# Kernel optimization log

Hardware: AMD Instinct MI355X
Metric: run time of the kernel (lower is better)

Reference implementation:

```python
import jax, jax.numpy as jnp
import numpy as np

H = 256; EMB = 256; MAX_POS = 20; NBOND = 4; ATOM = 40
DEPTH_T = 5; DEPTH_G = 5
NT, MT = 8000, 16000      # tree nodes / tree messages
NA, MA = 25000, 50000     # atoms / bond messages
NB = 6; NC = 12; NROOT = 256
VC, VI = 5000, 15000      # cluster / inter vocab sizes

FLOAT_KEYS = ("E_c","E_i","Wc_w","Wc_b","Wi_w","Wi_b","Wroot_w","Wroot_b",
  "t_Wo_w","t_Wo_b","t_Wz_w","t_Wz_b","t_Wr_w","t_Ur_w","t_Ur_b","t_Wh_w","t_Wh_b",
  "i_Wo_w","i_Wo_b","i_Wz_w","i_Wz_b","i_Wr_w","i_Ur_w","i_Ur_b","i_Wh_w","i_Wh_b",
  "g_Wo_w","g_Wo_b","g_Wz_w","g_Wz_b","g_Wr_w","g_Ur_w","g_Ur_b","g_Wh_w","g_Wh_b")
INT_KEYS = ("t_fnode","t_fmess","t_agraph","t_bgraph","t_cgraph",
            "g_fnode","g_fmess","g_agraph","g_bgraph","roots")

def _gru(fmess, bgraph, Wz_w, Wz_b, Wr_w, Ur_w, Ur_b, Wh_w, Wh_b, depth):
    # depth-iterated GRU message passing; row 0 of h is padding (kept at zero).
    M, F = fmess.shape
    Hs = Wz_w.shape[1]
    mask = jnp.ones((M, 1), fmess.dtype).at[0, 0].set(0.0)
    # loop-invariant input projections (W_z/W_h split along concat axis)
    fz = fmess @ Wz_w[:F] + Wz_b
    fr = fmess @ Wr_w
    fh = fmess @ Wh_w[:F] + Wh_b
    Wz_h, Wh_h = Wz_w[F:], Wh_w[F:]
    def step(h, _):
        h_nei = h[bgraph]                       # [M, B, H] irregular gather
        sum_h = h_nei.sum(1)
        z = jax.nn.sigmoid(fz + sum_h @ Wz_h)
        r = jax.nn.sigmoid(fr[:, None, :] + h_nei @ Ur_w + Ur_b)
        sum_gh = (r * h_nei).sum(1)
        pre_h = jnp.tanh(fh + sum_gh @ Wh_h)
        h_new = ((1.0 - z) * sum_h + z * pre_h) * mask
        return h_new, None
    h0 = jnp.zeros((M, Hs), fmess.dtype)
    h, _ = jax.lax.scan(step, h0, None, length=depth)
    return h

def _mpn(fnode, fmess, agraph, bgraph, p, depth):
    h = _gru(fmess, bgraph, p["Wz_w"], p["Wz_b"], p["Wr_w"], p["Ur_w"], p["Ur_b"], p["Wh_w"], p["Wh_b"], depth)
    nei = h[agraph].sum(1)                      # index_select_ND + sum
    nh = jax.nn.relu(jnp.concatenate([fnode, nei], 1) @ p["Wo_w"] + p["Wo_b"])
    return nh.at[0].set(0.0), h                 # zero padding row (mask)

def _enc_params(fl, pre):
    return {k: fl[pre + k] for k in ("Wo_w","Wo_b","Wz_w","Wz_b","Wr_w","Ur_w","Ur_b","Wh_w","Wh_b")}

def _forward(fl, it):
    E_pos = jnp.eye(MAX_POS, dtype=jnp.float32)
    E_a = jnp.eye(ATOM, dtype=jnp.float32)
    E_b = jnp.eye(NBOND, dtype=jnp.float32)
    t_fnode, t_fmess = it["t_fnode"], it["t_fmess"]
    g_fnode, g_fmess = it["g_fnode"], it["g_fmess"]
    # ---- embed_graph + graph_encoder ----
    g_hnode = E_a[g_fnode]                                           # [NA, ATOM] one-hot
    g_hmess = jnp.concatenate([g_hnode[g_fmess[:, 0]], E_b[g_fmess[:, 2]], E_pos[g_fmess[:, 3]]], 1)
    hatom, _ = _mpn(g_hnode, g_hmess, it["g_agraph"], it["g_bgraph"], _enc_params(fl, "g_"), DEPTH_G)
    # ---- embed_inter + inter_encoder ----
    fin = fl["E_i"][t_fnode[:, 1]]
    hn = hatom[it["t_cgraph"]].sum(1)                                # cluster <- atoms
    hn = jax.nn.relu(jnp.concatenate([fin, hn], 1) @ fl["Wi_w"] + fl["Wi_b"])
    hm = jnp.concatenate([hn[t_fmess[:, 0]], E_pos[t_fmess[:, 2]]], 1)
    hinter, _ = _mpn(hn, hm, it["t_agraph"], it["t_bgraph"], _enc_params(fl, "i_"), DEPTH_T)
    # ---- embed_tree + tree_encoder ----
    fin = fl["E_c"][t_fnode[:, 0]]
    hn = jax.nn.relu(jnp.concatenate([fin, hinter], 1) @ fl["Wc_w"] + fl["Wc_b"])
    hm = jnp.concatenate([hn[t_fmess[:, 0]], E_pos[t_fmess[:, 2]]], 1)
    htree, h_msg = _mpn(hn, hm, it["t_agraph"], it["t_bgraph"], _enc_params(fl, "t_"), DEPTH_T)
    # ---- embed_root: uses pre-encoder node embedding hn and message states h_msg ----
    r = it["roots"]
    nei = h_msg[it["t_agraph"][r]].sum(1)
    hroot = jnp.tanh(jnp.concatenate([hn[r], nei], 1) @ fl["Wroot_w"] + fl["Wroot_b"])
    return hroot, htree, hinter, hatom

def setup_inputs() -> dict:
    ki = iter(jax.random.split(jax.random.key(0), 80))
    def nk():
        return next(ki)
    ri = jax.random.randint
    rn = lambda shape: 0.08 * jax.random.normal(nk(), shape, jnp.float32)
    inp = {}
    inp["t_fnode"] = ri(nk(), (NT, 2), 0, VC)
    inp["t_fmess"] = jnp.stack([ri(nk(), (MT,), 0, NT), ri(nk(), (MT,), 0, NT), ri(nk(), (MT,), 0, MAX_POS)], 1)
    inp["t_agraph"] = ri(nk(), (NT, NB), 0, MT)
    inp["t_bgraph"] = ri(nk(), (MT, NB), 0, MT)
    inp["t_cgraph"] = ri(nk(), (NT, NC), 0, NA)
    inp["g_fnode"] = ri(nk(), (NA,), 0, ATOM)
    inp["g_fmess"] = jnp.stack([ri(nk(), (MA,), 0, NA), ri(nk(), (MA,), 0, NA), ri(nk(), (MA,), 0, NBOND), ri(nk(), (MA,), 0, MAX_POS)], 1)
    inp["g_agraph"] = ri(nk(), (NA, NB), 0, MA)
    inp["g_bgraph"] = ri(nk(), (MA, NB), 0, MA)
    inp["roots"] = ri(nk(), (NROOT,), 0, NT)
    inp["E_c"] = rn((VC, EMB)); inp["E_i"] = rn((VI, EMB))
    inp["Wc_w"] = rn((EMB + H, H)); inp["Wc_b"] = rn((H,))
    inp["Wi_w"] = rn((EMB + H, H)); inp["Wi_b"] = rn((H,))
    inp["Wroot_w"] = rn((2 * H, H)); inp["Wroot_b"] = rn((H,))
    for pre, in_sz, nf in (("t_", H + MAX_POS, H), ("i_", H + MAX_POS, H), ("g_", ATOM + NBOND + MAX_POS, ATOM)):
        inp[pre + "Wo_w"] = rn((nf + H, H)); inp[pre + "Wo_b"] = rn((H,))
        inp[pre + "Wz_w"] = rn((in_sz + H, H)); inp[pre + "Wz_b"] = rn((H,))
        inp[pre + "Wr_w"] = rn((in_sz, H))
        inp[pre + "Ur_w"] = rn((H, H)); inp[pre + "Ur_b"] = rn((H,))
        inp[pre + "Wh_w"] = rn((in_sz + H, H)); inp[pre + "Wh_b"] = rn((H,))
    return inp

def reference(E_c, E_i, Wc_w, Wc_b, Wi_w, Wi_b, Wroot_w, Wroot_b,
              t_Wo_w, t_Wo_b, t_Wz_w, t_Wz_b, t_Wr_w, t_Ur_w, t_Ur_b, t_Wh_w, t_Wh_b,
              i_Wo_w, i_Wo_b, i_Wz_w, i_Wz_b, i_Wr_w, i_Ur_w, i_Ur_b, i_Wh_w, i_Wh_b,
              g_Wo_w, g_Wo_b, g_Wz_w, g_Wz_b, g_Wr_w, g_Ur_w, g_Ur_b, g_Wh_w, g_Wh_b,
              t_fnode, t_fmess, t_agraph, t_bgraph, t_cgraph,
              g_fnode, g_fmess, g_agraph, g_bgraph, roots):
    a = dict(locals())
    fl = {k: a[k] for k in FLOAT_KEYS}
    it = {k: a[k] for k in INT_KEYS}
    return _forward(fl, it)
```

## Files before the change

kernel.cpp:

```cpp
#include <hip/hip_runtime.h>
#include <hip/hip_bf16.h>
#include <math.h>

typedef __hip_bfloat16 bf16;
typedef __attribute__((ext_vector_type(8))) short  bf16x8;
typedef __attribute__((ext_vector_type(4))) float  f32x4;

#define NT_ 8000
#define MT_ 16000
#define NA_ 25000
#define MA_ 50000
#define NROOT_ 256

struct Feat {
  const float* dtab; const int* didx; int dstride;
  const float* otab;
  const int* oidx0; int os0; int oo0;
  const int* oidx1; int os1; int oo1;
  const int* oidx2; int os2; int oo2;
  const float* bias;
};

__device__ __forceinline__ float rcpf_(float x){ return __builtin_amdgcn_rcpf(x); }
__device__ __forceinline__ float sigm(float x){ return rcpf_(1.0f + __expf(-x)); }
__device__ __forceinline__ float tanh_f(float x){
  float t = __expf(2.0f*x);
  return 1.0f - 2.0f*rcpf_(t + 1.0f);
}

__device__ __forceinline__ float ubf(unsigned int u){ union{unsigned int i; float f;} x; x.i = u<<16; return x.f; }
__device__ __forceinline__ unsigned int pack2bf(float a, float b){
  bf16 x = __float2bfloat16(a), y = __float2bfloat16(b);
  unsigned short ux = *(unsigned short*)&x, uy = *(unsigned short*)&y;
  return (unsigned int)ux | ((unsigned int)uy<<16);
}
__device__ __forceinline__ short f2bf_s(float f){
  bf16 b = __float2bfloat16(f);
  return *(short*)&b;
}
__device__ __forceinline__ float bfs2f(short s){ return ubf((unsigned short)s); }

__device__ __forceinline__ void acc4(float4& v, const float* p){
  float4 t = *(const float4*)p;
  v.x+=t.x; v.y+=t.y; v.z+=t.z; v.w+=t.w;
}
__device__ __forceinline__ float4 feat_eval4(const Feat& f, int m, int n){
  float4 v = make_float4(0,0,0,0);
  if (f.bias) acc4(v, f.bias + n);
  if (f.dtab) acc4(v, f.dtab + (size_t)f.didx[(size_t)m*f.dstride]*256 + n);
  if (f.otab){
    acc4(v, f.otab + (size_t)(f.oidx0[(size_t)m*f.os0]+f.oo0)*256 + n);
    if (f.oidx1) acc4(v, f.otab + (size_t)(f.oidx1[(size_t)m*f.os1]+f.oo1)*256 + n);
    if (f.oidx2) acc4(v, f.otab + (size_t)(f.oidx2[(size_t)m*f.os2]+f.oo2)*256 + n);
  }
  return v;
}
__device__ __forceinline__ float feat_eval(const Feat& f, int m, int n){
  float v = 0.0f;
  if (f.bias) v += f.bias[n];
  if (f.dtab) v += f.dtab[(size_t)f.didx[(size_t)m*f.dstride]*256 + n];
  if (f.otab){
    v += f.otab[((size_t)(f.oidx0[(size_t)m*f.os0]+f.oo0))*256 + n];
    if (f.oidx1) v += f.otab[((size_t)(f.oidx1[(size_t)m*f.os1]+f.oo1))*256 + n];
    if (f.oidx2) v += f.otab[((size_t)(f.oidx2[(size_t)m*f.os2]+f.oo2))*256 + n];
  }
  return v;
}

__global__ void k_aidx(const int* __restrict__ g_fnode, const int* __restrict__ g_fmess,
                       int* __restrict__ aidx, int M){
  int m = blockIdx.x*blockDim.x + threadIdx.x;
  if (m<M) aidx[m] = g_fnode[g_fmess[(size_t)m*4]];
}

struct SJob { const float* src; short* dst; int nrow; int pad; };
struct SJobs { SJob j[26]; };
__global__ void k_splitw_b(SJobs js){
  SJob jb = js.j[blockIdx.y];
  int idx = blockIdx.x*256 + threadIdx.x;
  if (idx >= jb.nrow*256) return;
  int k = idx>>8, n = idx&255;
  float w = jb.src[idx];
  int base = (((k>>5)*16 + (n>>4))<<10) + (((n&15) + (((k>>3)&3)<<4))<<4) + (k&7);
  short h = f2bf_s(w);
  jb.dst[base]   = h;
  jb.dst[base+8] = f2bf_s(w - bfs2f(h));
}

__global__ void k_gsum4(const float* __restrict__ src, const int* __restrict__ idx,
                        const int* __restrict__ rowsel, int J, int istride,
                        float* __restrict__ dst, int M){
  int wid = (blockIdx.x<<2) + (threadIdx.x>>6);
  if (wid>=M) return;
  int c = (threadIdx.x&63)<<2;
  int r = rowsel ? rowsel[wid] : wid;
  float4 s = make_float4(0,0,0,0);
  for (int j=0;j<J;j++){
    int id = idx[(size_t)r*istride+j];
    acc4(s, src + (size_t)id*256 + c);
  }
  *(float4*)(dst + (size_t)wid*256 + c) = s;
}

__device__ __forceinline__ void build_a(const float* p, bf16x8& hi, bf16x8& lo){
  float4 v0 = *(const float4*)p;
  float4 v1 = *(const float4*)(p+4);
  float vv[8]={v0.x,v0.y,v0.z,v0.w,v1.x,v1.y,v1.z,v1.w};
  #pragma unroll
  for (int j=0;j<8;j++){
    short h = f2bf_s(vv[j]);
    hi[j]=h;
    lo[j]=f2bf_s(vv[j]-bfs2f(h));
  }
}

#define MFMA __builtin_amdgcn_mfma_f32_16x16x32_bf16

__global__ __launch_bounds__(256)
void mfma_mm(const float* __restrict__ A, const short* __restrict__ Bp,
             float* __restrict__ outf, int M)
{
  const int tid=threadIdx.x, lane=tid&63, wc=tid>>6;
  const int rbase = blockIdx.x<<5;
  const int r0 = rbase + (lane&15), r1 = r0 + 16;
  const int koff = (lane>>4)<<3;
  f32x4 zero = {0.f,0.f,0.f,0.f};
  f32x4 acc[2][4];
  #pragma unroll
  for (int rf=0;rf<2;rf++)
    #pragma unroll
    for (int t=0;t<4;t++) acc[rf][t]=zero;

  for (int kc=0;kc<8;kc++){
    bf16x8 a0h={0,0,0,0,0,0,0,0}, a0l=a0h, a1h=a0h, a1l=a0h;
    if (r0<M) build_a(A + (size_t)r0*256 + kc*32 + koff, a0h, a0l);
    if (r1<M) build_a(A + (size_t)r1*256 + kc*32 + koff, a1h, a1l);
    #pragma unroll
    for (int t=0;t<4;t++){
      const short* p = Bp + (((kc<<4)+(wc<<2)+t)<<10) + (lane<<4);
      bf16x8 bh = *(const bf16x8*)p;
      bf16x8 bl = *(const bf16x8*)(p+8);
      acc[0][t]=MFMA(a0h,bh,acc[0][t],0,0,0);
      acc[1][t]=MFMA(a1h,bh,acc[1][t],0,0,0);
      acc[0][t]=MFMA(a0l,bh,acc[0][t],0,0,0);
      acc[1][t]=MFMA(a1l,bh,acc[1][t],0,0,0);
      acc[0][t]=MFMA(a0h,bl,acc[0][t],0,0,0);
      acc[1][t]=MFMA(a1h,bl,acc[1][t],0,0,0);
    }
  }
  const int rr = rbase + ((lane>>4)<<2);
  const int cl = lane&15;
  #pragma unroll
  for (int rf=0;rf<2;rf++)
    #pragma unroll
    for (int t=0;t<4;t++){
      int col = (((wc<<2)+t)<<4) + cl;
      #pragma unroll
      for (int r=0;r<4;r++){
        int m = rr + rf*16 + r;
        if (m<M) outf[(size_t)m*256+col] = acc[rf][t][r];
      }
    }
}

template<int NG>
__global__ __launch_bounds__(256)
void mfma_proj(const float* __restrict__ A1, const int* __restrict__ a1idx, int a1s,
               const float* __restrict__ A2,
               const short* __restrict__ B1p, const short* __restrict__ B2p,
               float* __restrict__ outf, float* __restrict__ outf2,
               Feat f1, int mask0, int M)
{
  const int tid=threadIdx.x, lane=tid&63, wc=tid>>6;
  const int rbase = blockIdx.x<<5;
  const int r0 = rbase + (lane&15), r1 = r0 + 16;
  const int koff = (lane>>4)<<3;
  const float* p0 = (r0<M) ? A1 + (size_t)(a1idx? a1idx[(size_t)r0*a1s] : r0)*256 : nullptr;
  const float* p1 = (r1<M) ? A1 + (size_t)(a1idx? a1idx[(size_t)r1*a1s] : r1)*256 : nullptr;
  f32x4 zero = {0.f,0.f,0.f,0.f};
  f32x4 acc[2][4];
  #pragma unroll
  for (int rf=0;rf<2;rf++)
    #pragma unroll
    for (int t=0;t<4;t++) acc[rf][t]=zero;

  for (int kc=0;kc<8;kc++){
    bf16x8 a0h={0,0,0,0,0,0,0,0}, a0l=a0h, a1h=a0h, a1l=a0h;
    bf16x8 c0h=a0h, c0l=a0h, c1h=a0h, c1l=a0h;
    if (p0) build_a(p0 + kc*32 + koff, a0h, a0l);
    if (p1) build_a(p1 + kc*32 + koff, a1h, a1l);
    if (NG==2){
      if (r0<M) build_a(A2 + (size_t)r0*256 + kc*32 + koff, c0h, c0l);
      if (r1<M) build_a(A2 + (size_t)r1*256 + kc*32 + koff, c1h, c1l);
    }
    #pragma unroll
    for (int t=0;t<4;t++){
      const short* p = B1p + (((kc<<4)+(wc<<2)+t)<<10) + (lane<<4);
      bf16x8 bh = *(const bf16x8*)p;
      bf16x8 bl = *(const bf16x8*)(p+8);
      acc[0][t]=MFMA(a0h,bh,acc[0][t],0,0,0);
      acc[1][t]=MFMA(a1h,bh,acc[1][t],0,0,0);
      acc[0][t]=MFMA(a0l,bh,acc[0][t],0,0,0);
      acc[1][t]=MFMA(a1l,bh,acc[1][t],0,0,0);
      acc[0][t]=MFMA(a0h,bl,acc[0][t],0,0,0);
      acc[1][t]=MFMA(a1h,bl,acc[1][t],0,0,0);
      if (NG==2){
        const short* q = B2p + (((kc<<4)+(wc<<2)+t)<<10) + (lane<<4);
        bf16x8 dh = *(const bf16x8*)q;
        bf16x8 dl = *(const bf16x8*)(q+8);
        acc[0][t]=MFMA(c0h,dh,acc[0][t],0,0,0);
        acc[1][t]=MFMA(c1h,dh,acc[1][t],0,0,0);
        acc[0][t]=MFMA(c0l,dh,acc[0][t],0,0,0);
        acc[1][t]=MFMA(c1l,dh,acc[1][t],0,0,0);
        acc[0][t]=MFMA(c0h,dl,acc[0][t],0,0,0);
        acc[1][t]=MFMA(c1h,dl,acc[1][t],0,0,0);
      }
    }
  }
  const int rr = rbase + ((lane>>4)<<2);
  const int cl = lane&15;
  #pragma unroll
  for (int rf=0;rf<2;rf++)
    #pragma unroll
    for (int t=0;t<4;t++){
      int col = (((wc<<2)+t)<<4) + cl;
      #pragma unroll
      for (int r=0;r<4;r++){
        int m = rr + rf*16 + r;
        if (m>=M) continue;
        float v = acc[rf][t][r] + feat_eval(f1, m, col);
        v = fmaxf(v, 0.0f);
        if (mask0 && m==0) v = 0.0f;
        outf[(size_t)m*256+col] = v;
        if (outf2) outf2[(size_t)m*256+col] = v;
      }
    }
}

__global__ __launch_bounds__(256)
void k_step1hu(Feat fz, Feat fh, const short* __restrict__ Bu,
               float* __restrict__ hout, bf16* __restrict__ hUout, int M)
{
  __shared__ short Hs[32][264];
  const int tid=threadIdx.x, lane=tid&63, wc=tid>>6;
  const int rbase = blockIdx.x<<5;
  const int rr = (lane>>4)<<2;
  const int cl = lane&15;
  const int koff = (lane>>4)<<3;

  #pragma unroll
  for (int rf=0;rf<2;rf++)
    #pragma unroll
    for (int t=0;t<4;t++){
      int col = (((wc<<2)+t)<<4) + cl;
      #pragma unroll
      for (int r=0;r<4;r++){
        int lrow = rr + rf*16 + r;
        int m = rbase + lrow;
        float v = 0.f;
        if (m<M && m!=0)
          v = sigm(feat_eval(fz,m,col))*tanh_f(feat_eval(fh,m,col));
        if (m<M) hout[(size_t)m*256+col]=v;
        Hs[lrow][col]=f2bf_s(v);
      }
    }
  __syncthreads();
  const int r0l = lane&15, r1l = r0l+16;
  f32x4 zero = {0.f,0.f,0.f,0.f};
  f32x4 acc[2][4];
  #pragma unroll
  for (int rf=0;rf<2;rf++)
    #pragma unroll
    for (int t=0;t<4;t++) acc[rf][t]=zero;
  for (int kc=0;kc<8;kc++){
    bf16x8 a0 = *(const bf16x8*)&Hs[r0l][kc*32+koff];
    bf16x8 a1 = *(const bf16x8*)&Hs[r1l][kc*32+koff];
    #pragma unroll
    for (int t=0;t<4;t++){
      const short* p = Bu + (((kc<<4)+(wc<<2)+t)<<10) + (lane<<4);
      bf16x8 bh = *(const bf16x8*)p;
      bf16x8 bl = *(const bf16x8*)(p+8);
      acc[0][t]=MFMA(a0,bh,acc[0][t],0,0,0);
      acc[1][t]=MFMA(a1,bh,acc[1][t],0,0,0);
      acc[0][t]=MFMA(a0,bl,acc[0][t],0,0,0);
      acc[1][t]=MFMA(a1,bl,acc[1][t],0,0,0);
    }
  }
  #pragma unroll
  for (int rf=0;rf<2;rf++)
    #pragma unroll
    for (int t=0;t<4;t++){
      int col = (((wc<<2)+t)<<4) + cl;
      #pragma unroll
      for (int r=0;r<4;r++){
        int m = rbase + rr + rf*16 + r;
        if (m<M) hUout[(size_t)m*256+col] = __float2bfloat16(acc[rf][t][r]);
      }
    }
}

template<int GEXT, int DO_HU>
__global__ __launch_bounds__(256)
void mfma_gg(const float* __restrict__ hprev, const bf16* __restrict__ hUprev,
             const int* __restrict__ bgraph, Feat fr,
             const short* __restrict__ Bz, const short* __restrict__ Bh,
             const short* __restrict__ Bze, const short* __restrict__ Bhe,
             const int* __restrict__ aidx, const int* __restrict__ gfm,
             const float* __restrict__ bzb, const float* __restrict__ bhb,
             Feat fz, Feat fh, const short* __restrict__ Bu,
             float* __restrict__ hout, bf16* __restrict__ hUout, int M)
{
  __shared__ float SH[32][260];
  __shared__ short SG[32][264];
  const int tid=threadIdx.x, lane=tid&63, wc=tid>>6;
  const int rbase = blockIdx.x<<5;
  const int koff = (lane>>4)<<3;

  {
    const int c = lane<<2;
    for (int s=0;s<8;s++){
      int lrow = (wc<<3) + s;
      int m = rbase + lrow;
      float4 sv = make_float4(0,0,0,0);
      float4 gv = make_float4(0,0,0,0);
      if (m < M){
        float4 fr4 = feat_eval4(fr, m, c);
        const int* bg = bgraph + (size_t)m*6;
        #pragma unroll
        for (int j=0;j<6;j++){
          int id = bg[j];
          float4 h4 = *(const float4*)(hprev + (size_t)id*256 + c);
          uint2  u2 = *(const uint2*)(hUprev + (size_t)id*256 + c);
          float u0=ubf(u2.x&0xffffu), u1=ubf(u2.x>>16);
          float u2f=ubf(u2.y&0xffffu), u3=ubf(u2.y>>16);
          sv.x+=h4.x; sv.y+=h4.y; sv.z+=h4.z; sv.w+=h4.w;
          gv.x += sigm(fr4.x+u0 )*h4.x;
          gv.y += sigm(fr4.y+u1 )*h4.y;
          gv.z += sigm(fr4.z+u2f)*h4.z;
          gv.w += sigm(fr4.w+u3 )*h4.w;
        }
      }
      *(float4*)&SH[lrow][c] = sv;
      uint2 p; p.x = pack2bf(gv.x,gv.y); p.y = pack2bf(gv.z,gv.w);
      *(uint2*)&SG[lrow][c] = p;
    }
  }
  __syncthreads();

  const int r0l = lane&15, r1l = r0l+16;
  const int r0 = rbase + r0l, r1 = rbase + r1l;
  f32x4 zero = {0.f,0.f,0.f,0.f};
  f32x4 accz[2][4], acch[2][4];
  #pragma unroll
  for (int rf=0;rf<2;rf++)
    #pragma unroll
    for (int t=0;t<4;t++){ accz[rf][t]=zero; acch[rf][t]=zero; }

  for (int kc=0;kc<8;kc++){
    bf16x8 a0h, a0l, a1h, a1l;
    build_a(&SH[r0l][kc*32+koff], a0h, a0l);
    build_a(&SH[r1l][kc*32+koff], a1h, a1l);
    bf16x8 s0 = *(const bf16x8*)&SG[r0l][kc*32+koff];
    bf16x8 s1 = *(const bf16x8*)&SG[r1l][kc*32+koff];
    #pragma unroll
    for (int t=0;t<4;t++){
      const short* pz = Bz + (((kc<<4)+(wc<<2)+t)<<10) + (lane<<4);
      const short* ph = Bh + (((kc<<4)+(wc<<2)+t)<<10) + (lane<<4);
      bf16x8 bzh = *(const bf16x8*)pz;
      bf16x8 bzl = *(const bf16x8*)(pz+8);
      bf16x8 bhh = *(const bf16x8*)ph;
      bf16x8 bhl = *(const bf16x8*)(ph+8);
      accz[0][t]=MFMA(a0h,bzh,accz[0][t],0,0,0);
      accz[1][t]=MFMA(a1h,bzh,accz[1][t],0,0,0);
      accz[0][t]=MFMA(a0l,bzh,accz[0][t],0,0,0);
      accz[1][t]=MFMA(a1l,bzh,accz[1][t],0,0,0);
      accz[0][t]=MFMA(a0h,bzl,accz[0][t],0,0,0);
      accz[1][t]=MFMA(a1h,bzl,accz[1][t],0,0,0);
      acch[0][t]=MFMA(s0,bhh,acch[0][t],0,0,0);
      acch[1][t]=MFMA(s1,bhh,acch[1][t],0,0,0);
      acch[0][t]=MFMA(s0,bhl,acch[0][t],0,0,0);
      acch[1][t]=MFMA(s1,bhl,acch[1][t],0,0,0);
    }
  }

  if (GEXT){
    int h0a=-1,h0b=-1,h0c=-1,h1a=-1,h1b=-1,h1c=-1;
    if (r0<M){ h0a=aidx[r0]; h0b=40+gfm[(size_t)r0*4+2]; h0c=44+gfm[(size_t)r0*4+3]; }
    if (r1<M){ h1a=aidx[r1]; h1b=40+gfm[(size_t)r1*4+2]; h1c=44+gfm[(size_t)r1*4+3]; }
    #pragma unroll
    for (int e=0;e<2;e++){
      bf16x8 ax0, ax1;
      #pragma unroll
      for (int j=0;j<8;j++){
        int d = e*32 + koff + j;
        ax0[j] = (d==h0a||d==h0b||d==h0c) ? (short)0x3F80 : (short)0;
        ax1[j] = (d==h1a||d==h1b||d==h1c) ? (short)0x3F80 : (short)0;
      }
      #pragma unroll
      for (int t=0;t<4;t++){
        const short* pe = Bze + (((e<<4)+(wc<<2)+t)<<10) + (lane<<4);
        const short* qe = Bhe + (((e<<4)+(wc<<2)+t)<<10) + (lane<<4);
        bf16x8 bzeh = *(const bf16x8*)pe;
        bf16x8 bzel = *(const bf16x8*)(pe+8);
        bf16x8 bheh = *(const bf16x8*)qe;
        bf16x8 bhel = *(const bf16x8*)(qe+8);
        accz[0][t]=MFMA(ax0,bzeh,accz[0][t],0,0,0);
        accz[1][t]=MFMA(ax1,bzeh,accz[1][t],0,0,0);
        accz[0][t]=MFMA(ax0,bzel,accz[0][t],0,0,0);
        accz[1][t]=MFMA(ax1,bzel,accz[1][t],0,0,0);
        acch[0][t]=MFMA(ax0,bheh,acch[0][t],0,0,0);
        acch[1][t]=MFMA(ax1,bheh,acch[1][t],0,0,0);
        acch[0][t]=MFMA(ax0,bhel,acch[0][t],0,0,0);
        acch[1][t]=MFMA(ax1,bhel,acch[1][t],0,0,0);
      }
    }
  }

  __syncthreads();

  const int rr = (lane>>4)<<2;
  const int cl = lane&15;
  #pragma unroll
  for (int rf=0;rf<2;rf++)
    #pragma unroll
    for (int t=0;t<4;t++){
      int col = (((wc<<2)+t)<<4) + cl;
      float fzb=0.f, fhb=0.f;
      if (GEXT){ fzb = bzb[col]; fhb = bhb[col]; }
      #pragma unroll
      for (int r=0;r<4;r++){
        int lrow = rr + rf*16 + r;
        int m = rbase + lrow;
        float v = 0.f;
        if (m<M){
          float fzv = GEXT ? fzb : feat_eval(fz,m,col);
          float fhv = GEXT ? fhb : feat_eval(fh,m,col);
          float z   = sigm  (accz[rf][t][r] + fzv);
          float pre = tanh_f(acch[rf][t][r] + fhv);
          float sh  = SH[lrow][col];
          v = (m==0) ? 0.f : ((1.f-z)*sh + z*pre);
          hout[(size_t)m*256+col] = v;
        }
        if (DO_HU) SG[lrow][col] = f2bf_s(v);
      }
    }

  if (DO_HU){
    __syncthreads();
    f32x4 acc[2][4];
    #pragma unroll
    for (int rf=0;rf<2;rf++)
      #pragma unroll
      for (int t=0;t<4;t++) acc[rf][t]=zero;
    for (int kc=0;kc<8;kc++){
      bf16x8 a0 = *(const bf16x8*)&SG[r0l][kc*32+koff];
      bf16x8 a1 = *(const bf16x8*)&SG[r1l][kc*32+koff];
      #pragma unroll
      for (int t=0;t<4;t++){
        const short* p = Bu + (((kc<<4)+(wc<<2)+t)<<10) + (lane<<4);
        bf16x8 bh = *(const bf16x8*)p;
        bf16x8 bl = *(const bf16x8*)(p+8);
        acc[0][t]=MFMA(a0,bh,acc[0][t],0,0,0);
        acc[1][t]=MFMA(a1,bh,acc[1][t],0,0,0);
        acc[0][t]=MFMA(a0,bl,acc[0][t],0,0,0);
        acc[1][t]=MFMA(a1,bl,acc[1][t],0,0,0);
      }
    }
    #pragma unroll
    for (int rf=0;rf<2;rf++)
      #pragma unroll
      for (int t=0;t<4;t++){
        int col = (((wc<<2)+t)<<4) + cl;
        #pragma unroll
        for (int r=0;r<4;r++){
          int m = rbase + rr + rf*16 + r;
          if (m<M) hUout[(size_t)m*256+col] = __float2bfloat16(acc[rf][t][r]);
        }
      }
  }
}

template<int NG, int MODE>
__global__ __launch_bounds__(256)
void gemm256(const float* __restrict__ A1, const float* __restrict__ B1,
             const float* __restrict__ A2, const float* __restrict__ B2,
             float* __restrict__ Cf, int M, Feat f1, int mask0)
{
  __shared__ float As[NG][16][36];
  __shared__ float Bs[NG][16][260];
  const int tid = threadIdx.x;
  const int bm = blockIdx.x<<5;
  const int tm = (tid>>5)<<2;
  const int c0 = (tid&31)<<2;

  float acc[NG][4][8];
  #pragma unroll
  for (int g=0;g<NG;g++)
    #pragma unroll
    for (int i=0;i<4;i++)
      #pragma unroll
      for (int j=0;j<8;j++) acc[g][i][j]=0.f;

  const int t7  = tid & 127;
  const int alm = t7>>2;
  const int alk = (t7&3)<<2;
  const int arow = bm + alm;
  const int amat = (NG==2)? (tid>>7) : 0;
  const bool astage = (NG==2) || (tid<128);

  for (int k0=0;k0<256;k0+=16){
    float a0=0,a1=0,a2=0,a3=0;
    if (astage && arow<M){
      const float* src = (amat==0)? A1 : A2;
      float4 v = *(const float4*)(src + (size_t)arow*256 + k0 + alk);
      a0=v.x; a1=v.y; a2=v.z; a3=v.w;
    }
    float4 breg[NG][4];
    #pragma unroll
    for (int g=0; g<NG; g++){
      const float* B = (g==0)? B1 : B2;
      #pragma unroll
      for (int j=0;j<4;j++){
        int slot = tid + 256*j;
        int kb = slot>>6, nb = (slot&63)<<2;
        breg[g][j] = *(const float4*)(B + (size_t)(k0+kb)*256 + nb);
      }
    }
    __syncthreads();
    if (astage){
      As[amat][alk+0][alm]=a0; As[amat][alk+1][alm]=a1;
      As[amat][alk+2][alm]=a2; As[amat][alk+3][alm]=a3;
    }
    #pragma unroll
    for (int g=0; g<NG; g++){
      #pragma unroll
      for (int j=0;j<4;j++){
        int slot = tid + 256*j;
        int kb = slot>>6, nb = (slot&63)<<2;
        *(float4*)&Bs[g][kb][nb] = breg[g][j];
      }
    }
    __syncthreads();
    #pragma unroll
    for (int k=0;k<16;k++){
      #pragma unroll
      for (int g=0;g<NG;g++){
        float4 av = *(const float4*)&As[g][k][tm];
        float4 b0 = *(const float4*)&Bs[g][k][c0];
        float4 b1 = *(const float4*)&Bs[g][k][c0+128];
        float a_[4]={av.x,av.y,av.z,av.w};
        float b_[8]={b0.x,b0.y,b0.z,b0.w,b1.x,b1.y,b1.z,b1.w};
        #pragma unroll
        for (int i=0;i<4;i++)
          #pragma unroll
          for (int j=0;j<8;j++)
            acc[g][i][j] = fmaf(a_[i], b_[j], acc[g][i][j]);
      }
    }
  }

  #pragma unroll
  for (int i=0;i<4;i++){
    int m = bm + tm + i;
    if (m >= M) continue;
    #pragma unroll
    for (int half=0; half<2; half++){
      int c = c0 + half*128;
      float4 r;
      float* rr = &r.x;
      float4 ft = feat_eval4(f1, m, c);
      float fv[4]={ft.x,ft.y,ft.z,ft.w};
      #pragma unroll
      for (int j=0;j<4;j++){
        float s = acc[0][i][half*4+j] + (NG>1?acc[1][i][half*4+j]:0.f) + fv[j];
        float v = (MODE==1)? fmaxf(s,0.f) : tanhf(s);
        if (MODE==1 && mask0 && m==0) v = 0.f;
        rr[j] = v;
      }
      *(float4*)(Cf + (size_t)m*256+c) = r;
    }
  }
}

extern "C" void kernel_launch(void* const* d_in, const int* in_sizes, int n_in,
                              void* d_out, int out_size, void* d_ws, size_t ws_size,
                              hipStream_t stream)
{
  const int* t_fnode  = (const int*)d_in[0];
  const int* t_fmess  = (const int*)d_in[1];
  const int* t_agraph = (const int*)d_in[2];
  const int* t_bgraph = (const int*)d_in[3];
  const int* t_cgraph = (const int*)d_in[4];
  const int* g_fnode  = (const int*)d_in[5];
  const int* g_fmess  = (const int*)d_in[6];
  const int* g_agraph = (const int*)d_in[7];
  const int* g_bgraph = (const int*)d_in[8];
  const int* roots    = (const int*)d_in[9];
  const float* E_c     = (const float*)d_in[10];
  const float* E_i     = (const float*)d_in[11];
  const float* Wc_w    = (const float*)d_in[12];
  const float* Wc_b    = (const float*)d_in[13];
  const float* Wi_w    = (const float*)d_in[14];
  const float* Wi_b    = (const float*)d_in[15];
  const float* Wroot_w = (const float*)d_in[16];
  const float* Wroot_b = (const float*)d_in[17];
  const float* t_Wo_w  = (const float*)d_in[18];
  const float* t_Wo_b  = (const float*)d_in[19];
  const float* t_Wz_w  = (const float*)d_in[20];
  const float* t_Wz_b  = (const float*)d_in[21];
  const float* t_Wr_w  = (const float*)d_in[22];
  const float* t_Ur_w  = (const float*)d_in[23];
  const float* t_Ur_b  = (const float*)d_in[24];
  const float* t_Wh_w  = (const float*)d_in[25];
  const float* t_Wh_b  = (const float*)d_in[26];
  const float* i_Wo_w  = (const float*)d_in[27];
  const float* i_Wo_b  = (const float*)d_in[28];
  const float* i_Wz_w  = (const float*)d_in[29];
  const float* i_Wz_b  = (const float*)d_in[30];
  const float* i_Wr_w  = (const float*)d_in[31];
  const float* i_Ur_w  = (const float*)d_in[32];
  const float* i_Ur_b  = (const float*)d_in[33];
  const float* i_Wh_w  = (const float*)d_in[34];
  const float* i_Wh_b  = (const float*)d_in[35];
  const float* g_Wo_w  = (const float*)d_in[36];
  const float* g_Wo_b  = (const float*)d_in[37];
  const float* g_Wz_w  = (const float*)d_in[38];
  const float* g_Wz_b  = (const float*)d_in[39];
  const float* g_Wr_w  = (const float*)d_in[40];
  const float* g_Ur_w  = (const float*)d_in[41];
  const float* g_Ur_b  = (const float*)d_in[42];
  const float* g_Wh_w  = (const float*)d_in[43];
  const float* g_Wh_b  = (const float*)d_in[44];

  float* out        = (float*)d_out;
  float* out_hroot  = out;
  float* out_htree  = out + (size_t)65536;
  float* out_hinter = out + (size_t)65536 + 2048000;
  float* out_hatom  = out + (size_t)65536 + 2048000 + 2048000;

  char* base = (char*)d_ws;
  int*   aidx   = (int*)base;
  short* SP     = (short*)(base + 262144);
  float* hbuf   = (float*)(base + 262144 + 8388608);
  float* hbufB  = hbuf + (size_t)12800000;
  bf16*  hUbuf  = (bf16*)(hbufB + (size_t)12800000);
  bf16*  hUbufB = hUbuf + (size_t)12800000;

  auto GP = [&](int i)->short* { return SP + (size_t)i*131072; };
  short* EZ = SP + (size_t)9*131072;
  short* EH = EZ + 32768;
  auto HP = [&](int j)->short* { return EH + 32768 + (size_t)j*131072; };
  short* P2 = EH + 32768 + (size_t)6*131072;
  auto PP = [&](int j)->short* { return P2 + (size_t)j*131072; };

  float* neibG    = hbufB;
  float* hatom    = hbufB + (size_t)25000*256;
  float* neib_t   = hbuf;
  float* hn_i     = hbuf  + (size_t)16000*256;
  float* hnWz     = hbufB + (size_t)16000*256;
  float* hnWr     = hbufB + (size_t)24000*256;
  float* hnWh     = hbufB + (size_t)32000*256;
  float* nei_i    = hbufB;
  float* hinter   = hbufB + (size_t)8000*256;
  float* hn_t     = hbuf  + (size_t)32000*256;
  float* nei_t    = hbufB;
  float* hn_roots = hbufB + (size_t)8000*256;
  float* nei_root = hbufB + (size_t)8256*256;

  (void)in_sizes; (void)n_in; (void)out_size; (void)ws_size;

  SJobs js;
  js.j[0]  = { g_Ur_w,                    GP(0), 256, 0 };
  js.j[1]  = { g_Wz_w + (size_t)64*256,   GP(1), 256, 0 };
  js.j[2]  = { g_Wh_w + (size_t)64*256,   GP(2), 256, 0 };
  js.j[3]  = { i_Ur_w,                    GP(3), 256, 0 };
  js.j[4]  = { i_Wz_w + (size_t)276*256,  GP(4), 256, 0 };
  js.j[5]  = { i_Wh_w + (size_t)276*256,  GP(5), 256, 0 };
  js.j[6]  = { t_Ur_w,                    GP(6), 256, 0 };
  js.j[7]  = { t_Wz_w + (size_t)276*256,  GP(7), 256, 0 };
  js.j[8]  = { t_Wh_w + (size_t)276*256,  GP(8), 256, 0 };
  js.j[9]  = { g_Wz_w,                    EZ,     64, 0 };
  js.j[10] = { g_Wh_w,                    EH,     64, 0 };
  js.j[11] = { i_Wz_w,                    HP(0), 256, 0 };
  js.j[12] = { i_Wr_w,                    HP(1), 256, 0 };
  js.j[13] = { i_Wh_w,                    HP(2), 256, 0 };
  js.j[14] = { t_Wz_w,                    HP(3), 256, 0 };
  js.j[15] = { t_Wr_w,                    HP(4), 256, 0 };
  js.j[16] = { t_Wh_w,                    HP(5), 256, 0 };
  js.j[17] = { Wi_w,                      PP(0), 256, 0 };
  js.j[18] = { Wi_w + (size_t)256*256,    PP(1), 256, 0 };
  js.j[19] = { Wc_w,                      PP(2), 256, 0 };
  js.j[20] = { Wc_w + (size_t)256*256,    PP(3), 256, 0 };
  js.j[21] = { i_Wo_w,                    PP(4), 256, 0 };
  js.j[22] = { i_Wo_w + (size_t)256*256,  PP(5), 256, 0 };
  js.j[23] = { t_Wo_w,                    PP(6), 256, 0 };
  js.j[24] = { t_Wo_w + (size_t)256*256,  PP(7), 256, 0 };
  js.j[25] = { g_Wo_w + (size_t)40*256,   PP(8), 256, 0 };
  k_splitw_b<<<dim3(256,26),256,0,stream>>>(js);

  Feat fzg{}; fzg.otab=g_Wz_w; fzg.oidx0=aidx;      fzg.os0=1; fzg.oo0=0;
              fzg.oidx1=g_fmess+2; fzg.os1=4; fzg.oo1=40;
              fzg.oidx2=g_fmess+3; fzg.os2=4; fzg.oo2=44; fzg.bias=g_Wz_b;
  Feat frg = fzg; frg.otab=g_Wr_w; frg.bias=g_Ur_b;
  Feat fhg = fzg; fhg.otab=g_Wh_w; fhg.bias=g_Wh_b;

  Feat fzi{}; fzi.dtab=hnWz; fzi.didx=t_fmess; fzi.dstride=3;
              fzi.otab=i_Wz_w; fzi.oidx0=t_fmess+2; fzi.os0=3; fzi.oo0=256; fzi.bias=i_Wz_b;
  Feat fri = fzi; fri.dtab=hnWr; fri.otab=i_Wr_w; fri.bias=i_Ur_b;
  Feat fhi = fzi; fhi.dtab=hnWh; fhi.otab=i_Wh_w; fhi.bias=i_Wh_b;

  Feat fzt = fzi; fzt.otab=t_Wz_w; fzt.bias=t_Wz_b;
  Feat frt = fri; frt.otab=t_Wr_w; frt.bias=t_Ur_b;
  Feat fht = fhi; fht.otab=t_Wh_w; fht.bias=t_Wh_b;

  Feat fnone{};

  auto run_gru = [&](int M, const int* bgraph, int p, bool gext,
                     Feat fz, Feat fr, Feat fh)->float* {
    int gb32 = (M+31)/32;
    const short* Bu = GP(p*3+0);
    const short* Bz = GP(p*3+1);
    const short* Bh = GP(p*3+2);
    k_step1hu<<<gb32,256,0,stream>>>(fz, fh, Bu, hbuf, hUbuf, M);
    float* hA = hbuf;  bf16* uA = hUbuf;
    float* hB = hbufB; bf16* uB = hUbufB;
    for (int d=0; d<4; ++d){
      if (d<3){
        if (gext)
          mfma_gg<1,1><<<gb32,256,0,stream>>>(hA, uA, bgraph, fr, Bz, Bh,
              EZ, EH, aidx, g_fmess, g_Wz_b, g_Wh_b, fnone, fnone, Bu, hB, uB, M);
        else
          mfma_gg<0,1><<<gb32,256,0,stream>>>(hA, uA, bgraph, fr, Bz, Bh,
              nullptr,nullptr,nullptr,nullptr,nullptr,nullptr, fz, fh, Bu, hB, uB, M);
      } else {
        if (gext)
          mfma_gg<1,0><<<gb32,256,0,stream>>>(hA, uA, bgraph, fr, Bz, Bh,
              EZ, EH, aidx, g_fmess, g_Wz_b, g_Wh_b, fnone, fnone, nullptr, hB, nullptr, M);
        else
          mfma_gg<0,0><<<gb32,256,0,stream>>>(hA, uA, bgraph, fr, Bz, Bh,
              nullptr,nullptr,nullptr,nullptr,nullptr,nullptr, fz, fh, nullptr, hB, nullptr, M);
      }
      float* th=hA; hA=hB; hB=th;
      bf16*  tu=uA; uA=uB; uB=tu;
    }
    return hA;
  };

  k_aidx<<<(MA_+255)/256,256,0,stream>>>(g_fnode, g_fmess, aidx, MA_);
  float* hg = run_gru(MA_, g_bgraph, 0, true, fzg, frg, fhg);
  k_gsum4<<<(NA_+3)/4,256,0,stream>>>(hg, g_agraph, nullptr, 6, 6, neibG, NA_);
  Feat fWo{}; fWo.otab=g_Wo_w; fWo.oidx0=g_fnode; fWo.os0=1; fWo.oo0=0; fWo.bias=g_Wo_b;
  mfma_proj<1><<<(NA_+31)/32,256,0,stream>>>(neibG, nullptr, 1, nullptr,
      PP(8), nullptr, hatom, out_hatom, fWo, 1, NA_);

  k_gsum4<<<(NT_+3)/4,256,0,stream>>>(hatom, t_cgraph, nullptr, 12, 12, neib_t, NT_);
  Feat fbWi{}; fbWi.bias=Wi_b;
  mfma_proj<2><<<NT_/32,256,0,stream>>>(E_i, t_fnode+1, 2, neib_t,
      PP(0), PP(1), hn_i, nullptr, fbWi, 0, NT_);
  mfma_mm<<<NT_/32,256,0,stream>>>(hn_i, HP(0), hnWz, NT_);
  mfma_mm<<<NT_/32,256,0,stream>>>(hn_i, HP(1), hnWr, NT_);
  mfma_mm<<<NT_/32,256,0,stream>>>(hn_i, HP(2), hnWh, NT_);

  float* hi = run_gru(MT_, t_bgraph, 1, false, fzi, fri, fhi);
  k_gsum4<<<(NT_+3)/4,256,0,stream>>>(hi, t_agraph, nullptr, 6, 6, nei_i, NT_);
  Feat fbWoi{}; fbWoi.bias=i_Wo_b;
  mfma_proj<2><<<NT_/32,256,0,stream>>>(hn_i, nullptr, 1, nei_i,
      PP(4), PP(5), hinter, out_hinter, fbWoi, 1, NT_);

  Feat fbWc{}; fbWc.bias=Wc_b;
  mfma_proj<2><<<NT_/32,256,0,stream>>>(E_c, t_fnode, 2, hinter,
      PP(2), PP(3), hn_t, nullptr, fbWc, 0, NT_);
  mfma_mm<<<NT_/32,256,0,stream>>>(hn_t, HP(3), hnWz, NT_);
  mfma_mm<<<NT_/32,256,0,stream>>>(hn_t, HP(4), hnWr, NT_);
  mfma_mm<<<NT_/32,256,0,stream>>>(hn_t, HP(5), hnWh, NT_);

  float* ht = run_gru(MT_, t_bgraph, 2, false, fzt, frt, fht);
  k_gsum4<<<(NT_+3)/4,256,0,stream>>>(ht, t_agraph, nullptr, 6, 6, nei_t, NT_);
  Feat fbWot{}; fbWot.bias=t_Wo_b;
  mfma_proj<2><<<NT_/32,256,0,stream>>>(hn_t, nullptr, 1, nei_t,
      PP(6), PP(7), out_htree, nullptr, fbWot, 1, NT_);

  k_gsum4<<<(NROOT_+3)/4,256,0,stream>>>(hn_t, roots, nullptr, 1, 1, hn_roots, NROOT_);
  k_gsum4<<<(NROOT_+3)/4,256,0,stream>>>(ht, t_agraph, roots, 6, 6, nei_root, NROOT_);
  Feat fbWr{}; fbWr.bias=Wroot_b;
  gemm256<2,2><<<NROOT_/32,256,0,stream>>>(hn_roots, Wroot_w, nei_root,
      Wroot_w + (size_t)256*256, out_hroot, NROOT_, fbWr, 0);
}
```

Before: 2.213 ms.

## Raise wave priority around MFMA loops and hoist feature index loads in GRU epilogue

Wraps the MFMA inner loops of several kernels in s_setprio high/low so waves doing matrix work get issue priority over waves in load or epilogue phases. In the non-GEXT mfma_gg epilogue, the per-row feature indices are loaded once into registers instead of being recomputed through feat_eval for every column. It also partially unrolls a gather loop. The index hoist assumes the fz and fh features share the same index arrays and only use one offset table, and it adds register pressure.

```diff
diff --git a/kernel.cpp b/kernel.cpp
--- a/kernel.cpp
+++ b/kernel.cpp
@@ -115,6 +115,8 @@
 }
 
 #define MFMA __builtin_amdgcn_mfma_f32_16x16x32_bf16
+#define PRIO_HI __builtin_amdgcn_s_setprio(1)
+#define PRIO_LO __builtin_amdgcn_s_setprio(0)
 
 __global__ __launch_bounds__(256)
 void mfma_mm(const float* __restrict__ A, const short* __restrict__ Bp,
@@ -131,6 +133,7 @@
     #pragma unroll
     for (int t=0;t<4;t++) acc[rf][t]=zero;
 
+  PRIO_HI;
   for (int kc=0;kc<8;kc++){
     bf16x8 a0h={0,0,0,0,0,0,0,0}, a0l=a0h, a1h=a0h, a1l=a0h;
     if (r0<M) build_a(A + (size_t)r0*256 + kc*32 + koff, a0h, a0l);
@@ -148,6 +151,7 @@
       acc[1][t]=MFMA(a1h,bl,acc[1][t],0,0,0);
     }
   }
+  PRIO_LO;
   const int rr = rbase + ((lane>>4)<<2);
   const int cl = lane&15;
   #pragma unroll
@@ -184,6 +188,7 @@
     #pragma unroll
     for (int t=0;t<4;t++) acc[rf][t]=zero;
 
+  PRIO_HI;
   for (int kc=0;kc<8;kc++){
     bf16x8 a0h={0,0,0,0,0,0,0,0}, a0l=a0h, a1h=a0h, a1l=a0h;
     bf16x8 c0h=a0h, c0l=a0h, c1h=a0h, c1l=a0h;
@@ -217,6 +222,7 @@
       }
     }
   }
+  PRIO_LO;
   const int rr = rbase + ((lane>>4)<<2);
   const int cl = lane&15;
   #pragma unroll
@@ -272,6 +278,7 @@
   for (int rf=0;rf<2;rf++)
     #pragma unroll
     for (int t=0;t<4;t++) acc[rf][t]=zero;
+  PRIO_HI;
   for (int kc=0;kc<8;kc++){
     bf16x8 a0 = *(const bf16x8*)&Hs[r0l][kc*32+koff];
     bf16x8 a1 = *(const bf16x8*)&Hs[r1l][kc*32+koff];
@@ -286,6 +293,7 @@
       acc[1][t]=MFMA(a1,bl,acc[1][t],0,0,0);
     }
   }
+  PRIO_LO;
   #pragma unroll
   for (int rf=0;rf<2;rf++)
     #pragma unroll
@@ -318,6 +326,7 @@
 
   {
     const int c = lane<<2;
+    #pragma unroll 2
     for (int s=0;s<8;s++){
       int lrow = (wc<<3) + s;
       int m = rbase + lrow;
@@ -356,6 +365,7 @@
     #pragma unroll
     for (int t=0;t<4;t++){ accz[rf][t]=zero; acch[rf][t]=zero; }
 
+  PRIO_HI;
   for (int kc=0;kc<8;kc++){
     bf16x8 a0h, a0l, a1h, a1l;
     build_a(&SH[r0l][kc*32+koff], a0h, a0l);
@@ -415,11 +425,24 @@
       }
     }
   }
+  PRIO_LO;
 
   __syncthreads();
 
   const int rr = (lane>>4)<<2;
   const int cl = lane&15;
+  int src8[8], pos8[8];
+  if (!GEXT){
+    #pragma unroll
+    for (int rf=0;rf<2;rf++)
+      #pragma unroll
+      for (int r=0;r<4;r++){
+        int m = rbase + rr + rf*16 + r;
+        int mm = (m<M)? m : 0;
+        src8[rf*4+r] = fz.didx [(size_t)mm*fz.dstride];
+        pos8[rf*4+r] = fz.oidx0[(size_t)mm*fz.os0] + fz.oo0;
+      }
+  }
   #pragma unroll
   for (int rf=0;rf<2;rf++)
     #pragma unroll
@@ -433,8 +456,15 @@
         int m = rbase + lrow;
         float v = 0.f;
         if (m<M){
-          float fzv = GEXT ? fzb : feat_eval(fz,m,col);
-          float fhv = GEXT ? fhb : feat_eval(fh,m,col);
+          float fzv, fhv;
+          if (GEXT){ fzv = fzb; fhv = fhb; }
+          else {
+            int i8 = rf*4+r;
+            size_t so = (size_t)src8[i8]*256 + col;
+            size_t po = (size_t)pos8[i8]*256 + col;
+            fzv = fz.bias[col] + fz.dtab[so] + fz.otab[po];
+            fhv = fh.bias[col] + fh.dtab[so] + fh.otab[po];
+          }
           float z   = sigm  (accz[rf][t][r] + fzv);
           float pre = tanh_f(acch[rf][t][r] + fhv);
           float sh  = SH[lrow][col];
@@ -452,6 +482,7 @@
     for (int rf=0;rf<2;rf++)
       #pragma unroll
       for (int t=0;t<4;t++) acc[rf][t]=zero;
+    PRIO_HI;
     for (int kc=0;kc<8;kc++){
       bf16x8 a0 = *(const bf16x8*)&SG[r0l][kc*32+koff];
       bf16x8 a1 = *(const bf16x8*)&SG[r1l][kc*32+koff];
@@ -466,6 +497,7 @@
         acc[1][t]=MFMA(a1,bl,acc[1][t],0,0,0);
       }
     }
+    PRIO_LO;
     #pragma unroll
     for (int rf=0;rf<2;rf++)
       #pragma unroll
```

Measured after the change: 1.858 ms (median of 2 runs). 16.0% less time.
